# Optimization experiments

Measured on AMD Instinct MI355X. Metric: run time of the kernel, lower is better.

## Reference

```python
import jax, jax.numpy as jnp
import numpy as np

N = 100000   # nodes
E = 1250000  # edges
R = 8        # num_relations
D = 64       # in_channels = hidden = out dim (all 64 per RGIN_Net construction)
L = 2        # max_depth
EPS = 1e-5


def setup_inputs() -> dict:
    key = jax.random.key(0)
    ks = jax.random.split(key, 18)
    s = 1.0 / np.sqrt(D)
    inp = {
        'x': jax.random.normal(ks[0], (N, D), dtype=jnp.float32),
        'edge_index': jax.random.randint(ks[1], (2, E), 0, N, dtype=jnp.int64),
        'edge_type': jax.random.randint(ks[2], (E,), 0, R, dtype=jnp.int64),
        # per-relation MLP params, stacked over L layers and R relations
        'W1': jax.random.normal(ks[3], (L, R, D, D), dtype=jnp.float32) * s,
        'b1': jax.random.normal(ks[4], (L, R, D), dtype=jnp.float32) * 0.01,
        'g1': 1.0 + 0.1 * jax.random.normal(ks[5], (L, R, D), dtype=jnp.float32),
        'be1': jax.random.normal(ks[6], (L, R, D), dtype=jnp.float32) * 0.01,
        'W2': jax.random.normal(ks[7], (L, R, D, D), dtype=jnp.float32) * s,
        'b2': jax.random.normal(ks[8], (L, R, D), dtype=jnp.float32) * 0.01,
        # root MLP params per layer
        'rW1': jax.random.normal(ks[9], (L, D, D), dtype=jnp.float32) * s,
        'rb1': jax.random.normal(ks[10], (L, D), dtype=jnp.float32) * 0.01,
        'rg1': 1.0 + 0.1 * jax.random.normal(ks[11], (L, D), dtype=jnp.float32),
        'rbe1': jax.random.normal(ks[12], (L, D), dtype=jnp.float32) * 0.01,
        'rW2': jax.random.normal(ks[13], (L, D, D), dtype=jnp.float32) * s,
        'rb2': jax.random.normal(ks[14], (L, D), dtype=jnp.float32) * 0.01,
        'bias': jax.random.normal(ks[15], (L, D), dtype=jnp.float32) * 0.01,
    }
    return inp


def _bn(z, gamma, beta, axis):
    # BatchNorm1d in training mode: batch stats, biased variance
    mean = jnp.mean(z, axis=axis, keepdims=True)
    var = jnp.mean(jnp.square(z - mean), axis=axis, keepdims=True)
    return (z - mean) * jax.lax.rsqrt(var + EPS) * gamma + beta


def _forward(x, edge_index, edge_type, W1, b1, g1, be1, W2, b2,
             rW1, rb1, rg1, rbe1, rW2, rb2, bias):
    src, dst = edge_index[0], edge_index[1]
    # combined segment id encodes (relation, dst-node) -> one fused scatter-add
    seg = edge_type * N + dst
    for i in range(L):
        # gather -> scatter-add per relation: h[r, n] = sum_{e: type=r, dst=n} x[src[e]]
        h = jax.ops.segment_sum(x[src], seg, num_segments=R * N).reshape(R, N, D)
        # per-relation MLP: Linear -> BN -> ReLU -> Linear (summed over relations)
        z = jnp.einsum('rnd,rdh->rnh', h, W1[i]) + b1[i][:, None, :]
        z = jax.nn.relu(_bn(z, g1[i][:, None, :], be1[i][:, None, :], axis=1))
        rel = jnp.einsum('rnh,rho->rno', z, W2[i]) + b2[i][:, None, :]
        out = rel.sum(axis=0)
        # root MLP on x itself
        zr = x @ rW1[i] + rb1[i]
        zr = jax.nn.relu(_bn(zr, rg1[i], rbe1[i], axis=0))
        out = out + zr @ rW2[i] + rb2[i] + bias[i]
        x = jax.nn.relu(out) if i + 1 < L else out  # dropout p=0.0
    return x


def reference(x, edge_index, edge_type, W1, b1, g1, be1, W2, b2,
              rW1, rb1, rg1, rbe1, rW2, rb2, bias):
    return _forward(x, edge_index, edge_type, W1, b1, g1, be1, W2, b2,
                    rW1, rb1, rg1, rbe1, rW2, rb2, bias)
```

## Files before the change

### kernel.cpp

```cpp
#include <hip/hip_runtime.h>

#define NN 100000
#define NE 1250000
#define NR 8
#define DD 64
#define TILE 128
#define NTILES 782
#define NBUCKETS (NR * NTILES)
#define CAP 512
#define HROW 72
#define EPSB 1e-5f

typedef unsigned short u16;
typedef unsigned int u32;
typedef __attribute__((ext_vector_type(8))) short short8;
typedef __attribute__((ext_vector_type(4))) float f32x4;

static __device__ __forceinline__ float b2f_lo(u32 v) { return __uint_as_float(v << 16); }
static __device__ __forceinline__ float b2f_hi(u32 v) { return __uint_as_float(v & 0xffff0000u); }
static __device__ __forceinline__ u16 f2b(float f) {
    u32 u = __float_as_uint(f);
    u += 0x7fffu + ((u >> 16) & 1u);
    return (u16)(u >> 16);
}
static __device__ __forceinline__ u32 pk(float a, float b) {
    return (u32)f2b(a) | ((u32)f2b(b) << 16);
}
static __device__ __forceinline__ void acc8(float* acc, uint4 v0, uint4 v1, uint4 v2, uint4 v3) {
#pragma unroll
    for (int q = 0; q < 4; q++) {
        uint4 v = (q == 0) ? v0 : (q == 1) ? v1 : (q == 2) ? v2 : v3;
        acc[q * 8 + 0] += b2f_lo(v.x);
        acc[q * 8 + 1] += b2f_hi(v.x);
        acc[q * 8 + 2] += b2f_lo(v.y);
        acc[q * 8 + 3] += b2f_hi(v.y);
        acc[q * 8 + 4] += b2f_lo(v.z);
        acc[q * 8 + 5] += b2f_hi(v.z);
        acc[q * 8 + 6] += b2f_lo(v.w);
        acc[q * 8 + 7] += b2f_hi(v.w);
    }
}


__global__ void cvt_kernel(const float* __restrict__ in, u16* __restrict__ outb) {
    int i = blockIdx.x * 256 + threadIdx.x;
    if (i < NN * DD / 8) {
        float4 a = *(const float4*)&in[i * 8];
        float4 b = *(const float4*)&in[i * 8 + 4];
        uint4 o;
        o.x = pk(a.x, a.y); o.y = pk(a.z, a.w);
        o.z = pk(b.x, b.y); o.w = pk(b.z, b.w);
        *(uint4*)&outb[i * 8] = o;
    }
}


__global__ void wt_kernel(const float* __restrict__ W1, const float* __restrict__ rW1,
                          const float* __restrict__ W2, const float* __restrict__ rW2,
                          u16* __restrict__ wt1g, u16* __restrict__ wt2g) {
    int m = blockIdx.x;
    int i = m / 18, rest = m % 18;
    int set = rest / 9, r = rest % 9;
    const float* W = (set == 0)
        ? ((r < NR) ? (W1 + ((size_t)i * NR + r) * DD * DD) : (rW1 + (size_t)i * DD * DD))
        : ((r < NR) ? (W2 + ((size_t)i * NR + r) * DD * DD) : (rW2 + (size_t)i * DD * DD));
    u32* dst = (u32*)((set == 0 ? wt1g : wt2g) + ((size_t)i * 9 + r) * DD * DD);
    for (int j = threadIdx.x; j < DD * 32; j += 256) {
        int d = j >> 5, kp = j & 31;
        dst[j] = pk(W[(2 * kp) * DD + d], W[(2 * kp + 1) * DD + d]);
    }
}


__global__ void count_kernel(const int* __restrict__ dst,
                             const int* __restrict__ et,
                             int* __restrict__ cnt) {
    int i = blockIdx.x * 256 + threadIdx.x;
    if (i < NE) atomicAdd(&cnt[et[i] * NTILES + (dst[i] >> 7)], 1);
}

__global__ void scan_kernel(const int* __restrict__ cnt, int* __restrict__ off, int n) {
    __shared__ int ts[1024];
    int t = threadIdx.x;
    int v[8];
    int s = 0;
#pragma unroll
    for (int j = 0; j < 8; j++) {
        int idx = t * 8 + j;
        int c = (idx < n) ? cnt[idx] : 0;
        v[j] = s;
        s += c;
    }
    ts[t] = s;
    __syncthreads();
    for (int d = 1; d < 1024; d <<= 1) {
        int add = (t >= d) ? ts[t - d] : 0;
        __syncthreads();
        ts[t] += add;
        __syncthreads();
    }
    int base = (t > 0) ? ts[t - 1] : 0;
#pragma unroll
    for (int j = 0; j < 8; j++) {
        int idx = t * 8 + j;
        if (idx < n) off[idx] = base + v[j];
    }
    if (t == 1023) off[n] = ts[1023];
}

__global__ void fill_kernel(const int* __restrict__ src, const int* __restrict__ dst,
                            const int* __restrict__ et, const int* __restrict__ off,
                            int* __restrict__ cursor, int* __restrict__ ep) {
    int i = blockIdx.x * 256 + threadIdx.x;
    if (i < NE) {
        int d = dst[i];
        int b = et[i] * NTILES + (d >> 7);
        int pos = off[b] + atomicAdd(&cursor[b], 1);
        ep[pos] = (src[i] << 8) | (d & 127);
    }
}


__launch_bounds__(256, 4)
__global__ void gemm1_kernel(const u16* __restrict__ xb,
                             const int* __restrict__ ep, const int* __restrict__ off,
                             const u16* __restrict__ wt1, const float* __restrict__ b1l,
                             const float* __restrict__ rb1l,
                             u16* __restrict__ zb, float* __restrict__ stats) {
    __shared__ u16 hsb[TILE * HROW];
    __shared__ int seS[CAP], seD[CAP];
    __shared__ int shist[TILE], scur[TILE];
    __shared__ int soff[TILE + 1];
    __shared__ float red[2 * DD];
    int r = blockIdx.y;
    bool root = (r == NR);
    int n0 = blockIdx.x * TILE;
    int tid = threadIdx.x;

    int wv = tid >> 6;
    int l  = tid & 63;
    int lr = l & 15;
    int lg = l >> 4;

    if (tid < 128) red[tid] = 0.f;

    if (!root) {
        int b = r * NTILES + blockIdx.x;
        int e0 = off[b], e1 = off[b + 1];
        int m = e1 - e0;
        int slot = tid & 127, half = tid >> 7;
        float acc[32];
#pragma unroll
        for (int j = 0; j < 32; j++) acc[j] = 0.f;

        for (int base = 0; base < m; base += CAP) {
            int cnt = min(m - base, CAP);
            if (tid < TILE) shist[tid] = 0;
            __syncthreads();
            for (int i = tid; i < cnt; i += 256) {
                int p = ep[e0 + base + i];
                seS[i] = p;
                atomicAdd(&shist[p & 127], 1);
            }
            __syncthreads();
            if (tid < 64) {
                int c0 = shist[tid], c1 = shist[tid + 64];
                int s0 = c0, s1 = c1;
#pragma unroll
                for (int d = 1; d < 64; d <<= 1) {
                    int t0 = __shfl_up(s0, d);
                    int t1 = __shfl_up(s1, d);
                    if (tid >= d) { s0 += t0; s1 += t1; }
                }
                int tot0 = __shfl(s0, 63);
                soff[tid + 1]  = s0;
                soff[tid + 65] = tot0 + s1;
                if (tid == 0) soff[0] = 0;
                scur[tid]      = s0 - c0;
                scur[tid + 64] = tot0 + s1 - c1;
            }
            __syncthreads();
            for (int i = tid; i < cnt; i += 256) {
                int p = seS[i];
                seD[atomicAdd(&scur[p & 127], 1)] = p;
            }
            __syncthreads();
            int sb = soff[slot], se = soff[slot + 1];
            int e = sb;
            for (; e + 2 <= se; e += 2) {
                const u16* xr0 = &xb[(size_t)(seD[e] >> 8) * DD + half * 32];
                const u16* xr1 = &xb[(size_t)(seD[e + 1] >> 8) * DD + half * 32];
                uint4 a0 = *(const uint4*)(xr0);      uint4 c0 = *(const uint4*)(xr1);
                uint4 a1 = *(const uint4*)(xr0 + 8);  uint4 c1 = *(const uint4*)(xr1 + 8);
                uint4 a2 = *(const uint4*)(xr0 + 16); uint4 c2 = *(const uint4*)(xr1 + 16);
                uint4 a3 = *(const uint4*)(xr0 + 24); uint4 c3 = *(const uint4*)(xr1 + 24);
                acc8(acc, a0, a1, a2, a3);
                acc8(acc, c0, c1, c2, c3);
            }
            if (e < se) {
                const u16* xr = &xb[(size_t)(seD[e] >> 8) * DD + half * 32];
                acc8(acc, *(const uint4*)(xr), *(const uint4*)(xr + 8),
                     *(const uint4*)(xr + 16), *(const uint4*)(xr + 24));
            }
        }
        u32 pw[16];
#pragma unroll
        for (int j = 0; j < 16; j++) pw[j] = pk(acc[2 * j], acc[2 * j + 1]);
        u16* hrow = &hsb[slot * HROW + half * 32];
        *(uint4*)(hrow)      = make_uint4(pw[0], pw[1], pw[2], pw[3]);
        *(uint4*)(hrow + 8)  = make_uint4(pw[4], pw[5], pw[6], pw[7]);
        *(uint4*)(hrow + 16) = make_uint4(pw[8], pw[9], pw[10], pw[11]);
        *(uint4*)(hrow + 24) = make_uint4(pw[12], pw[13], pw[14], pw[15]);
    } else {
        for (int idx = tid; idx < TILE * 8; idx += 256) {
            int row = idx >> 3, q = idx & 7;
            int n = n0 + row;
            uint4 v = make_uint4(0, 0, 0, 0);
            if (n < NN) v = *(const uint4*)&xb[(size_t)n * DD + q * 8];
            *(uint4*)&hsb[row * HROW + q * 8] = v;
        }
    }

    const u16* wtg = wt1 + (size_t)r * DD * DD;
    short8 bfrg[2][4];
#pragma unroll
    for (int ks = 0; ks < 2; ks++)
#pragma unroll
        for (int ct = 0; ct < 4; ct++)
            bfrg[ks][ct] = *(const short8*)&wtg[(ct * 16 + lr) * DD + ks * 32 + lg * 8];
    __syncthreads();

    f32x4 dacc[2][4];
#pragma unroll
    for (int rt = 0; rt < 2; rt++)
#pragma unroll
        for (int ct = 0; ct < 4; ct++) dacc[rt][ct] = (f32x4){0.f, 0.f, 0.f, 0.f};

#pragma unroll
    for (int ks = 0; ks < 2; ks++) {
        short8 afr[2];
#pragma unroll
        for (int rt = 0; rt < 2; rt++)
            afr[rt] = *(const short8*)&hsb[(wv * 32 + rt * 16 + lr) * HROW + ks * 32 + lg * 8];
#pragma unroll
        for (int ct = 0; ct < 4; ct++) {
            dacc[0][ct] = __builtin_amdgcn_mfma_f32_16x16x32_bf16(afr[0], bfrg[ks][ct], dacc[0][ct], 0, 0, 0);
            dacc[1][ct] = __builtin_amdgcn_mfma_f32_16x16x32_bf16(afr[1], bfrg[ks][ct], dacc[1][ct], 0, 0, 0);
        }
    }

    const float* bvec = root ? rb1l : (b1l + r * DD);
    float bv4[4], s1v[4], s2v[4];
#pragma unroll
    for (int ct = 0; ct < 4; ct++) { bv4[ct] = bvec[16 * ct + lr]; s1v[ct] = 0.f; s2v[ct] = 0.f; }
#pragma unroll
    for (int rt = 0; rt < 2; rt++)
#pragma unroll
        for (int ct = 0; ct < 4; ct++)
#pragma unroll
            for (int i = 0; i < 4; i++) {
                float v = dacc[rt][ct][i] + bv4[ct];
                dacc[rt][ct][i] = v;
                int n = n0 + wv * 32 + rt * 16 + lg * 4 + i;
                if (n < NN) { s1v[ct] += v; s2v[ct] += v * v; }
            }
#pragma unroll
    for (int ct = 0; ct < 4; ct++) {
        float a = s1v[ct], bq = s2v[ct];
        a += __shfl_xor(a, 16); bq += __shfl_xor(bq, 16);
        a += __shfl_xor(a, 32); bq += __shfl_xor(bq, 32);
        if (lg == 0) {
            atomicAdd(&red[16 * ct + lr], a);
            atomicAdd(&red[64 + 16 * ct + lr], bq);
        }
    }
    __syncthreads();

#pragma unroll
    for (int rt = 0; rt < 2; rt++)
#pragma unroll
        for (int ct = 0; ct < 4; ct++)
#pragma unroll
            for (int i = 0; i < 4; i++)
                hsb[(wv * 32 + rt * 16 + lg * 4 + i) * HROW + 16 * ct + lr] = f2b(dacc[rt][ct][i]);
    __syncthreads();

    u16* zout = zb + (size_t)r * NN * DD;
    for (int idx = tid; idx < TILE * 8; idx += 256) {
        int row = idx >> 3, q = idx & 7;
        int n = n0 + row;
        if (n < NN)
            *(uint4*)&zout[(size_t)n * DD + q * 8] = *(const uint4*)&hsb[row * HROW + q * 8];
    }
    if (tid < 64) {
        atomicAdd(&stats[r * DD + tid], red[tid]);
        atomicAdd(&stats[576 + r * DD + tid], red[64 + tid]);
    }
}


__global__ void finalize_kernel(const float* __restrict__ stats,
                                const float* __restrict__ g1l, const float* __restrict__ be1l,
                                const float* __restrict__ rg1l, const float* __restrict__ rbe1l,
                                const float* __restrict__ b2l, const float* __restrict__ rb2l,
                                const float* __restrict__ biasl,
                                float* __restrict__ affine, float* __restrict__ constd) {
    int t = threadIdx.x;
    if (t < 576) {
        int r = t >> 6, d = t & 63;
        float mean = stats[t] * (1.f / NN);
        float var = fmaxf(stats[576 + t] * (1.f / NN) - mean * mean, 0.f);
        float g  = (r < NR) ? g1l[r * DD + d]  : rg1l[d];
        float be = (r < NR) ? be1l[r * DD + d] : rbe1l[d];
        float sc = g * rsqrtf(var + EPSB);
        affine[t] = sc;
        affine[576 + t] = be - mean * sc;
        if (r == 0) {
            float cd = rb2l[d] + biasl[d];
#pragma unroll
            for (int rr = 0; rr < NR; rr++) cd += b2l[rr * DD + d];
            constd[d] = cd;
        }
    }
}


__launch_bounds__(256, 4)
__global__ void pass2_kernel(const u16* __restrict__ zb, const u16* __restrict__ wt2,
                             const float* __restrict__ affine, const float* __restrict__ constd,
                             float* __restrict__ outf, u16* __restrict__ outb,
                             int emit_bf16_relu) {
    __shared__ u16 zsb[TILE * HROW];
    __shared__ u16 wtb[DD * HROW];
    int n0 = blockIdx.x * TILE;
    int tid = threadIdx.x;
    int srow = tid >> 3;
    int sc0 = (tid & 7) * 8;

    int wv = tid >> 6;
    int l  = tid & 63;
    int lr = l & 15;
    int lg = l >> 4;

    f32x4 dacc[2][4];
#pragma unroll
    for (int rt = 0; rt < 2; rt++)
#pragma unroll
        for (int ct = 0; ct < 4; ct++) dacc[rt][ct] = (f32x4){0.f, 0.f, 0.f, 0.f};

    uint4 preA[4], preB[4];
    u32 wreg[8];
#pragma unroll
    for (int q = 0; q < 4; q++) {
        int n = n0 + srow + 32 * q;
        preA[q] = (n < NN) ? *(const uint4*)&zb[(size_t)n * DD + sc0] : make_uint4(0, 0, 0, 0);
        preB[q] = (n < NN) ? *(const uint4*)&zb[(size_t)NN * DD + (size_t)n * DD + sc0]
                           : make_uint4(0, 0, 0, 0);
    }
    {
        const u32* wsrc = (const u32*)wt2;
#pragma unroll
        for (int j = 0; j < 8; j++) wreg[j] = wsrc[tid + 256 * j];
    }

#pragma unroll
    for (int r = 0; r < 9; r++) {
        uint4* cur = (r & 1) ? preB : preA;
        float4 aLo = *(const float4*)&affine[r * DD + sc0];
        float4 aHi = *(const float4*)&affine[r * DD + sc0 + 4];
        float4 cLo = *(const float4*)&affine[576 + r * DD + sc0];
        float4 cHi = *(const float4*)&affine[576 + r * DD + sc0 + 4];
        __syncthreads();
#pragma unroll
        for (int q = 0; q < 4; q++) {
            uint4 vv = cur[q];
            float a0 = fmaxf(fmaf(b2f_lo(vv.x), aLo.x, cLo.x), 0.f);
            float a1 = fmaxf(fmaf(b2f_hi(vv.x), aLo.y, cLo.y), 0.f);
            float a2 = fmaxf(fmaf(b2f_lo(vv.y), aLo.z, cLo.z), 0.f);
            float a3 = fmaxf(fmaf(b2f_hi(vv.y), aLo.w, cLo.w), 0.f);
            float a4 = fmaxf(fmaf(b2f_lo(vv.z), aHi.x, cHi.x), 0.f);
            float a5 = fmaxf(fmaf(b2f_hi(vv.z), aHi.y, cHi.y), 0.f);
            float a6 = fmaxf(fmaf(b2f_lo(vv.w), aHi.z, cHi.z), 0.f);
            float a7 = fmaxf(fmaf(b2f_hi(vv.w), aHi.w, cHi.w), 0.f);
            uint4 o = make_uint4(pk(a0, a1), pk(a2, a3), pk(a4, a5), pk(a6, a7));
            *(uint4*)&zsb[(srow + 32 * q) * HROW + sc0] = o;
        }
        {
            int row = tid >> 5, q = tid & 31;
#pragma unroll
            for (int j = 0; j < 8; j++)
                ((u32*)&wtb[(row + 8 * j) * HROW])[q] = wreg[j];
        }
        __syncthreads();
        if (r + 1 < 9) {
            const u32* wsrc = (const u32*)(wt2 + (size_t)(r + 1) * DD * DD);
#pragma unroll
            for (int j = 0; j < 8; j++) wreg[j] = wsrc[tid + 256 * j];
        }
        if (r + 2 < 9) {
            const u16* zp = zb + (size_t)(r + 2) * NN * DD;
#pragma unroll
            for (int q = 0; q < 4; q++) {
                int n = n0 + srow + 32 * q;
                cur[q] = (n < NN) ? *(const uint4*)&zp[(size_t)n * DD + sc0]
                                  : make_uint4(0, 0, 0, 0);
            }
        }
#pragma unroll
        for (int ks = 0; ks < 2; ks++) {
            short8 afr[2];
#pragma unroll
            for (int rt = 0; rt < 2; rt++)
                afr[rt] = *(const short8*)&zsb[(wv * 32 + rt * 16 + lr) * HROW + ks * 32 + lg * 8];
#pragma unroll
            for (int ct = 0; ct < 4; ct++) {
                short8 bfr = *(const short8*)&wtb[(ct * 16 + lr) * HROW + ks * 32 + lg * 8];
                dacc[0][ct] = __builtin_amdgcn_mfma_f32_16x16x32_bf16(afr[0], bfr, dacc[0][ct], 0, 0, 0);
                dacc[1][ct] = __builtin_amdgcn_mfma_f32_16x16x32_bf16(afr[1], bfr, dacc[1][ct], 0, 0, 0);
            }
        }
    }

    float cd4[4];
#pragma unroll
    for (int ct = 0; ct < 4; ct++) cd4[ct] = constd[16 * ct + lr];

    if (emit_bf16_relu) {
        __syncthreads();
#pragma unroll
        for (int rt = 0; rt < 2; rt++)
#pragma unroll
            for (int ct = 0; ct < 4; ct++)
#pragma unroll
                for (int i = 0; i < 4; i++) {
                    float v = fmaxf(dacc[rt][ct][i] + cd4[ct], 0.f);
                    zsb[(wv * 32 + rt * 16 + lg * 4 + i) * HROW + 16 * ct + lr] = f2b(v);
                }
        __syncthreads();
        for (int idx = tid; idx < TILE * 8; idx += 256) {
            int row = idx >> 3, q = idx & 7;
            int n = n0 + row;
            if (n < NN)
                *(uint4*)&outb[(size_t)n * DD + q * 8] = *(const uint4*)&zsb[row * HROW + q * 8];
        }
    } else {
        float* zf = (float*)zsb;
#pragma unroll
        for (int h = 0; h < 2; h++) {
            __syncthreads();
#pragma unroll
            for (int rt = 0; rt < 2; rt++)
#pragma unroll
                for (int cc = 0; cc < 2; cc++) {
                    int ct = 2 * h + cc;
#pragma unroll
                    for (int i = 0; i < 4; i++)
                        zf[(wv * 32 + rt * 16 + lg * 4 + i) * 34 + 16 * cc + lr] =
                            dacc[rt][ct][i] + cd4[ct];
                }
            __syncthreads();
            for (int idx = tid; idx < TILE * 8; idx += 256) {
                int row = idx >> 3, q = idx & 7;
                int n = n0 + row;
                if (n < NN)
                    *(float4*)&outf[(size_t)n * DD + 32 * h + q * 4] =
                        *(const float4*)&zf[row * 34 + q * 4];
            }
        }
    }
}


extern "C" void kernel_launch(void* const* d_in, const int* in_sizes, int n_in,
                              void* d_out, int out_size, void* d_ws, size_t ws_size,
                              hipStream_t stream) {
    (void)in_sizes; (void)n_in; (void)out_size;

    const float* x0   = (const float*)d_in[0];
    const int*   ei   = (const int*)d_in[1];
    const int*   et   = (const int*)d_in[2];
    const float* W1   = (const float*)d_in[3];
    const float* b1   = (const float*)d_in[4];
    const float* g1   = (const float*)d_in[5];
    const float* be1  = (const float*)d_in[6];
    const float* W2   = (const float*)d_in[7];
    const float* b2   = (const float*)d_in[8];
    const float* rW1  = (const float*)d_in[9];
    const float* rb1  = (const float*)d_in[10];
    const float* rg1  = (const float*)d_in[11];
    const float* rbe1 = (const float*)d_in[12];
    const float* rW2  = (const float*)d_in[13];
    const float* rb2  = (const float*)d_in[14];
    const float* bias = (const float*)d_in[15];
    float* out = (float*)d_out;

    char* ws = (char*)d_ws;
    size_t zelems = (size_t)9 * NN * DD;
    u16* zb   = (u16*)ws;
    u16* xb   = zb + zelems;
    u16* wt1g = xb + (size_t)NN * DD;
    u16* wt2g = wt1g + 18 * DD * DD;
    float* stats  = (float*)(wt2g + 18 * DD * DD);
    float* affine = stats + 2304;
    float* constd = affine + 1152;
    int* cnt    = (int*)(constd + 64);
    int* cursor = cnt + NBUCKETS;
    int* off    = cursor + NBUCKETS;
    int* ep     = off + NBUCKETS + 1;

    size_t need = (zelems + (size_t)NN * DD + 36 * DD * DD) * 2
                + (2304 + 1152 + 64) * 4
                + ((size_t)3 * NBUCKETS + 1 + NE) * 4;
    if (ws_size < need) return;

    cvt_kernel<<<(NN * DD / 8 + 255) / 256, 256, 0, stream>>>(x0, xb);
    wt_kernel<<<36, 256, 0, stream>>>(W1, rW1, W2, rW2, wt1g, wt2g);
    hipMemsetAsync(cnt, 0, sizeof(int) * 2 * NBUCKETS, stream);
    hipMemsetAsync(stats, 0, sizeof(float) * 2304, stream);
    count_kernel<<<(NE + 255) / 256, 256, 0, stream>>>(ei + NE, et, cnt);
    scan_kernel<<<1, 1024, 0, stream>>>(cnt, off, NBUCKETS);
    fill_kernel<<<(NE + 255) / 256, 256, 0, stream>>>(ei, ei + NE, et, off, cursor, ep);

    for (int i = 0; i < 2; i++) {
        gemm1_kernel<<<dim3(NTILES, 9), 256, 0, stream>>>(
            xb, ep, off,
            wt1g + (size_t)i * 9 * DD * DD,
            b1 + (size_t)i * NR * DD, rb1 + (size_t)i * DD,
            zb, stats + (size_t)i * 1152);
        finalize_kernel<<<1, 576, 0, stream>>>(
            stats + (size_t)i * 1152,
            g1 + (size_t)i * NR * DD, be1 + (size_t)i * NR * DD,
            rg1 + (size_t)i * DD, rbe1 + (size_t)i * DD,
            b2 + (size_t)i * NR * DD, rb2 + (size_t)i * DD, bias + (size_t)i * DD,
            affine, constd);
        pass2_kernel<<<NTILES, 256, 0, stream>>>(
            zb, wt2g + (size_t)i * 9 * DD * DD,
            affine, constd, out, xb, (i == 0) ? 1 : 0);
    }
}
```

Measured before the change: 457.3 us.

## Double gemm1 block to 512 threads with four lanes per node row

Each gemm1 block now runs 512 threads instead of 256. In the gather phase each destination row is split across four threads holding 16 columns each, where before two threads held 32 columns each, and the inner edge loop is unrolled by four. In the MFMA phase each of the eight waves handles 16 rows instead of 32. The aim is to raise memory-level parallelism and occupancy for the latency-bound random gather and to cut register pressure. In exchange, shared-memory setup and the barrier and reduction work are spread over more threads, and each thread issues smaller loads per row.

```diff
diff --git a/kernel.cpp b/kernel.cpp
--- a/kernel.cpp
+++ b/kernel.cpp
@@ -26,19 +26,15 @@
 static __device__ __forceinline__ u32 pk(float a, float b) {
     return (u32)f2b(a) | ((u32)f2b(b) << 16);
 }
-static __device__ __forceinline__ void acc8(float* acc, uint4 v0, uint4 v1, uint4 v2, uint4 v3) {
-#pragma unroll
-    for (int q = 0; q < 4; q++) {
-        uint4 v = (q == 0) ? v0 : (q == 1) ? v1 : (q == 2) ? v2 : v3;
-        acc[q * 8 + 0] += b2f_lo(v.x);
-        acc[q * 8 + 1] += b2f_hi(v.x);
-        acc[q * 8 + 2] += b2f_lo(v.y);
-        acc[q * 8 + 3] += b2f_hi(v.y);
-        acc[q * 8 + 4] += b2f_lo(v.z);
-        acc[q * 8 + 5] += b2f_hi(v.z);
-        acc[q * 8 + 6] += b2f_lo(v.w);
-        acc[q * 8 + 7] += b2f_hi(v.w);
-    }
+static __device__ __forceinline__ void acc4(float* acc, uint4 v0, uint4 v1) {
+    acc[0]  += b2f_lo(v0.x); acc[1]  += b2f_hi(v0.x);
+    acc[2]  += b2f_lo(v0.y); acc[3]  += b2f_hi(v0.y);
+    acc[4]  += b2f_lo(v0.z); acc[5]  += b2f_hi(v0.z);
+    acc[6]  += b2f_lo(v0.w); acc[7]  += b2f_hi(v0.w);
+    acc[8]  += b2f_lo(v1.x); acc[9]  += b2f_hi(v1.x);
+    acc[10] += b2f_lo(v1.y); acc[11] += b2f_hi(v1.y);
+    acc[12] += b2f_lo(v1.z); acc[13] += b2f_hi(v1.z);
+    acc[14] += b2f_lo(v1.w); acc[15] += b2f_hi(v1.w);
 }
 
 
@@ -121,7 +117,7 @@
 }
 
 
-__launch_bounds__(256, 4)
+__launch_bounds__(512, 6)
 __global__ void gemm1_kernel(const u16* __restrict__ xb,
                              const int* __restrict__ ep, const int* __restrict__ off,
                              const u16* __restrict__ wt1, const float* __restrict__ b1l,
@@ -137,7 +133,7 @@
     int n0 = blockIdx.x * TILE;
     int tid = threadIdx.x;
 
-    int wv = tid >> 6;
+    int wv2 = tid >> 6;
     int l  = tid & 63;
     int lr = l & 15;
     int lg = l >> 4;
@@ -148,24 +144,25 @@
         int b = r * NTILES + blockIdx.x;
         int e0 = off[b], e1 = off[b + 1];
         int m = e1 - e0;
-        int slot = tid & 127, half = tid >> 7;
-        float acc[32];
-#pragma unroll
-        for (int j = 0; j < 32; j++) acc[j] = 0.f;
+        int slot = tid >> 2, quarter = tid & 3;
+        int c0 = quarter * 16;
+        float acc[16];
+#pragma unroll
+        for (int j = 0; j < 16; j++) acc[j] = 0.f;
 
         for (int base = 0; base < m; base += CAP) {
             int cnt = min(m - base, CAP);
             if (tid < TILE) shist[tid] = 0;
             __syncthreads();
-            for (int i = tid; i < cnt; i += 256) {
+            for (int i = tid; i < cnt; i += 512) {
                 int p = ep[e0 + base + i];
                 seS[i] = p;
                 atomicAdd(&shist[p & 127], 1);
             }
             __syncthreads();
             if (tid < 64) {
-                int c0 = shist[tid], c1 = shist[tid + 64];
-                int s0 = c0, s1 = c1;
+                int c0s = shist[tid], c1s = shist[tid + 64];
+                int s0 = c0s, s1 = c1s;
 #pragma unroll
                 for (int d = 1; d < 64; d <<= 1) {
                     int t0 = __shfl_up(s0, d);
@@ -176,43 +173,44 @@
                 soff[tid + 1]  = s0;
                 soff[tid + 65] = tot0 + s1;
                 if (tid == 0) soff[0] = 0;
-                scur[tid]      = s0 - c0;
-                scur[tid + 64] = tot0 + s1 - c1;
+                scur[tid]      = s0 - c0s;
+                scur[tid + 64] = tot0 + s1 - c1s;
             }
             __syncthreads();
-            for (int i = tid; i < cnt; i += 256) {
+            for (int i = tid; i < cnt; i += 512) {
                 int p = seS[i];
                 seD[atomicAdd(&scur[p & 127], 1)] = p;
             }
             __syncthreads();
             int sb = soff[slot], se = soff[slot + 1];
             int e = sb;
-            for (; e + 2 <= se; e += 2) {
-                const u16* xr0 = &xb[(size_t)(seD[e] >> 8) * DD + half * 32];
-                const u16* xr1 = &xb[(size_t)(seD[e + 1] >> 8) * DD + half * 32];
-                uint4 a0 = *(const uint4*)(xr0);      uint4 c0 = *(const uint4*)(xr1);
-                uint4 a1 = *(const uint4*)(xr0 + 8);  uint4 c1 = *(const uint4*)(xr1 + 8);
-                uint4 a2 = *(const uint4*)(xr0 + 16); uint4 c2 = *(const uint4*)(xr1 + 16);
-                uint4 a3 = *(const uint4*)(xr0 + 24); uint4 c3 = *(const uint4*)(xr1 + 24);
-                acc8(acc, a0, a1, a2, a3);
-                acc8(acc, c0, c1, c2, c3);
-            }
-            if (e < se) {
-                const u16* xr = &xb[(size_t)(seD[e] >> 8) * DD + half * 32];
-                acc8(acc, *(const uint4*)(xr), *(const uint4*)(xr + 8),
-                     *(const uint4*)(xr + 16), *(const uint4*)(xr + 24));
-            }
-        }
-        u32 pw[16];
-#pragma unroll
-        for (int j = 0; j < 16; j++) pw[j] = pk(acc[2 * j], acc[2 * j + 1]);
-        u16* hrow = &hsb[slot * HROW + half * 32];
-        *(uint4*)(hrow)      = make_uint4(pw[0], pw[1], pw[2], pw[3]);
-        *(uint4*)(hrow + 8)  = make_uint4(pw[4], pw[5], pw[6], pw[7]);
-        *(uint4*)(hrow + 16) = make_uint4(pw[8], pw[9], pw[10], pw[11]);
-        *(uint4*)(hrow + 24) = make_uint4(pw[12], pw[13], pw[14], pw[15]);
+            for (; e + 4 <= se; e += 4) {
+                const u16* x0p = &xb[(size_t)(seD[e]     >> 8) * DD + c0];
+                const u16* x1p = &xb[(size_t)(seD[e + 1] >> 8) * DD + c0];
+                const u16* x2p = &xb[(size_t)(seD[e + 2] >> 8) * DD + c0];
+                const u16* x3p = &xb[(size_t)(seD[e + 3] >> 8) * DD + c0];
+                uint4 a0 = *(const uint4*)(x0p), a1 = *(const uint4*)(x0p + 8);
+                uint4 b0 = *(const uint4*)(x1p), b1 = *(const uint4*)(x1p + 8);
+                uint4 cc0 = *(const uint4*)(x2p), cc1 = *(const uint4*)(x2p + 8);
+                uint4 d0 = *(const uint4*)(x3p), d1 = *(const uint4*)(x3p + 8);
+                acc4(acc, a0, a1);
+                acc4(acc, b0, b1);
+                acc4(acc, cc0, cc1);
+                acc4(acc, d0, d1);
+            }
+            for (; e < se; e++) {
+                const u16* xr = &xb[(size_t)(seD[e] >> 8) * DD + c0];
+                acc4(acc, *(const uint4*)(xr), *(const uint4*)(xr + 8));
+            }
+        }
+        u32 pw[8];
+#pragma unroll
+        for (int j = 0; j < 8; j++) pw[j] = pk(acc[2 * j], acc[2 * j + 1]);
+        u16* hrow = &hsb[slot * HROW + c0];
+        *(uint4*)(hrow)     = make_uint4(pw[0], pw[1], pw[2], pw[3]);
+        *(uint4*)(hrow + 8) = make_uint4(pw[4], pw[5], pw[6], pw[7]);
     } else {
-        for (int idx = tid; idx < TILE * 8; idx += 256) {
+        for (int idx = tid; idx < TILE * 8; idx += 512) {
             int row = idx >> 3, q = idx & 7;
             int n = n0 + row;
             uint4 v = make_uint4(0, 0, 0, 0);
@@ -230,23 +228,16 @@
             bfrg[ks][ct] = *(const short8*)&wtg[(ct * 16 + lr) * DD + ks * 32 + lg * 8];
     __syncthreads();
 
-    f32x4 dacc[2][4];
-#pragma unroll
-    for (int rt = 0; rt < 2; rt++)
-#pragma unroll
-        for (int ct = 0; ct < 4; ct++) dacc[rt][ct] = (f32x4){0.f, 0.f, 0.f, 0.f};
+    f32x4 dacc[4];
+#pragma unroll
+    for (int ct = 0; ct < 4; ct++) dacc[ct] = (f32x4){0.f, 0.f, 0.f, 0.f};
 
 #pragma unroll
     for (int ks = 0; ks < 2; ks++) {
-        short8 afr[2];
-#pragma unroll
-        for (int rt = 0; rt < 2; rt++)
-            afr[rt] = *(const short8*)&hsb[(wv * 32 + rt * 16 + lr) * HROW + ks * 32 + lg * 8];
-#pragma unroll
-        for (int ct = 0; ct < 4; ct++) {
-            dacc[0][ct] = __builtin_amdgcn_mfma_f32_16x16x32_bf16(afr[0], bfrg[ks][ct], dacc[0][ct], 0, 0, 0);
-            dacc[1][ct] = __builtin_amdgcn_mfma_f32_16x16x32_bf16(afr[1], bfrg[ks][ct], dacc[1][ct], 0, 0, 0);
-        }
+        short8 afr = *(const short8*)&hsb[(wv2 * 16 + lr) * HROW + ks * 32 + lg * 8];
+#pragma unroll
+        for (int ct = 0; ct < 4; ct++)
+            dacc[ct] = __builtin_amdgcn_mfma_f32_16x16x32_bf16(afr, bfrg[ks][ct], dacc[ct], 0, 0, 0);
     }
 
     const float* bvec = root ? rb1l : (b1l + r * DD);
@@ -254,16 +245,14 @@
 #pragma unroll
     for (int ct = 0; ct < 4; ct++) { bv4[ct] = bvec[16 * ct + lr]; s1v[ct] = 0.f; s2v[ct] = 0.f; }
 #pragma unroll
-    for (int rt = 0; rt < 2; rt++)
-#pragma unroll
-        for (int ct = 0; ct < 4; ct++)
-#pragma unroll
-            for (int i = 0; i < 4; i++) {
-                float v = dacc[rt][ct][i] + bv4[ct];
-                dacc[rt][ct][i] = v;
-                int n = n0 + wv * 32 + rt * 16 + lg * 4 + i;
-                if (n < NN) { s1v[ct] += v; s2v[ct] += v * v; }
-            }
+    for (int ct = 0; ct < 4; ct++)
+#pragma unroll
+        for (int i = 0; i < 4; i++) {
+            float v = dacc[ct][i] + bv4[ct];
+            dacc[ct][i] = v;
+            int n = n0 + wv2 * 16 + lg * 4 + i;
+            if (n < NN) { s1v[ct] += v; s2v[ct] += v * v; }
+        }
 #pragma unroll
     for (int ct = 0; ct < 4; ct++) {
         float a = s1v[ct], bq = s2v[ct];
@@ -277,16 +266,14 @@
     __syncthreads();
 
 #pragma unroll
-    for (int rt = 0; rt < 2; rt++)
-#pragma unroll
-        for (int ct = 0; ct < 4; ct++)
-#pragma unroll
-            for (int i = 0; i < 4; i++)
-                hsb[(wv * 32 + rt * 16 + lg * 4 + i) * HROW + 16 * ct + lr] = f2b(dacc[rt][ct][i]);
+    for (int ct = 0; ct < 4; ct++)
+#pragma unroll
+        for (int i = 0; i < 4; i++)
+            hsb[(wv2 * 16 + lg * 4 + i) * HROW + 16 * ct + lr] = f2b(dacc[ct][i]);
     __syncthreads();
 
     u16* zout = zb + (size_t)r * NN * DD;
-    for (int idx = tid; idx < TILE * 8; idx += 256) {
+    for (int idx = tid; idx < TILE * 8; idx += 512) {
         int row = idx >> 3, q = idx & 7;
         int n = n0 + row;
         if (n < NN)
@@ -522,7 +509,7 @@
     fill_kernel<<<(NE + 255) / 256, 256, 0, stream>>>(ei, ei + NE, et, off, cursor, ep);
 
     for (int i = 0; i < 2; i++) {
-        gemm1_kernel<<<dim3(NTILES, 9), 256, 0, stream>>>(
+        gemm1_kernel<<<dim3(NTILES, 9), 512, 0, stream>>>(
             xb, ep, off,
             wt1g + (size_t)i * 9 * DD * DD,
             b1 + (size_t)i * NR * DD, rb1 + (size_t)i * DD,
```

Result: slower. 563.3 us (+23.2%).
